# Kernel tuning notes

Hardware: AMD Instinct MI355X
Metric: run time of the kernel (lower is better)

Reference implementation:

```python
import jax, jax.numpy as jnp
import numpy as np

L, N, E, H, D = 2048, 4, 1024, 16, 128  # seq, batch, embed, heads, proj_dim
HD = E // H                             # head_dim = 64
SIGMA = 1.0
EPS = 1e-6


def setup_inputs() -> dict:
    key = jax.random.key(0)
    ks = jax.random.split(key, 13)
    w = lambda i, shape: jax.random.normal(ks[i], shape, jnp.float32) * 0.02
    return {
        "query": jax.random.normal(ks[0], (L, N, E), jnp.float32),
        "key": jax.random.normal(ks[1], (L, N, E), jnp.float32),
        "value": jax.random.normal(ks[2], (L, N, E), jnp.float32),
        "wq": w(3, (E, E)), "bq": jnp.zeros((E,), jnp.float32),
        "wk": w(4, (E, E)), "bk": jnp.zeros((E,), jnp.float32),
        "wv": w(5, (E, E)), "bv": jnp.zeros((E,), jnp.float32),
        "wo": w(6, (E, E)), "bo": jnp.zeros((E,), jnp.float32),
        "random_matrices": SIGMA * jax.random.normal(ks[7], (H, D, HD), jnp.float32),
    }


def random_project(x, rm):
    # x: (L, N, H, HD), rm: (H, D, HD) -> phi: (N*H, L, 2D)
    scale = 1.0 / np.sqrt(2 * D).astype(np.float32)
    xn = x / jnp.maximum(jnp.linalg.norm(x, axis=-1, keepdims=True), 1e-12)
    xt = jnp.einsum('lnhe,hde->lnhd', xn, rm)
    phi = scale * jnp.concatenate([jnp.exp(xt), jnp.exp(-xt)], axis=-1)  # (L,N,H,2D)
    # faithful to torch .contiguous().view(-1, L, 2D): plain row-major reshape
    return phi.reshape(N * H, L, 2 * D)


def causal_product(phi_q, phi_k, v):
    # phi_q, phi_k: (B, L, 2D); v: (B, L, HD)
    B = phi_q.shape[0]
    def step(carry, inp):
        S, z = carry            # S: (B, 2D, HD) running kv; z: (B, 2D) running k-sum
        qk, kk, vv = inp        # (B, 2D), (B, 2D), (B, HD)
        S = S + kk[:, :, None] * vv[:, None, :]
        z = z + kk
        num = jnp.einsum('bd,bdh->bh', qk, S)
        den = jnp.einsum('bd,bd->b', qk, z)
        return (S, z), num / (den[:, None] + EPS)
    init = (jnp.zeros((B, 2 * D, HD), phi_q.dtype), jnp.zeros((B, 2 * D), phi_q.dtype))
    xs = (jnp.swapaxes(phi_q, 0, 1), jnp.swapaxes(phi_k, 0, 1), jnp.swapaxes(v, 0, 1))
    _, out = jax.lax.scan(step, init, xs)   # out: (L, B, HD)
    return jnp.swapaxes(out, 0, 1)          # (B, L, HD)


def reference(query, key, value, wq, bq, wk, bk, wv, bv, wo, bo, random_matrices):
    q = query @ wq.T + bq
    k = key @ wk.T + bk
    v = value @ wv.T + bv
    q = q.reshape(L, N, H, HD)
    k = k.reshape(L, N, H, HD)
    v = jnp.swapaxes(v.reshape(L, N * H, HD), 0, 1)   # (B=N*H, L, HD)
    phi_q = random_project(q, random_matrices)        # (B, L, 2D)
    phi_k = random_project(k, random_matrices)
    attn = causal_product(phi_q, phi_k, v)            # (B, L, HD)
    attn = jnp.swapaxes(attn, 0, 1).reshape(L, N, E)
    return attn @ wo.T + bo
```

## Files before the change

### kernel.cpp

```cpp
#include <hip/hip_runtime.h>
#include <math.h>


typedef unsigned short u16;
typedef unsigned int u32;
using f32x4v  = __attribute__((ext_vector_type(4))) float;
using f32x16v = __attribute__((ext_vector_type(16))) float;
using s16x8   = __attribute__((ext_vector_type(8))) short;

__device__ __forceinline__ float bf2f(u16 u) { return __uint_as_float(((u32)u) << 16); }
__device__ __forceinline__ u16 f2bf(float x) {
    u32 b = __float_as_uint(x);
    b += 0x7fff + ((b >> 16) & 1);
    return (u16)(b >> 16);
}
__device__ __forceinline__ u32 cvtpk(float lo, float hi) {
    u32 r;
    asm("v_cvt_pk_bf16_f32 %0, %1, %2" : "=v"(r) : "v"(lo), "v"(hi));
    return r;
}
__device__ __forceinline__ float exp2f_hw(float x) {
    float r;
    asm("v_exp_f32 %0, %1" : "=v"(r) : "v"(x));
    return r;
}
__device__ __forceinline__ void gload_lds16(const void* g, void* l) {
    __builtin_amdgcn_global_load_lds(
        (const __attribute__((address_space(1))) void*)g,
        (__attribute__((address_space(3))) void*)l, 16, 0, 0);
}

__global__ __launch_bounds__(256) void cvt_consts(
    const float* __restrict__ w0, const float* __restrict__ w1,
    const float* __restrict__ w2, const float* __restrict__ w3,
    const float* __restrict__ rm, const float* __restrict__ query,
    const float* __restrict__ key, u16* __restrict__ wqkv,
    u16* __restrict__ wob, u16* __restrict__ rmb,
    u16* __restrict__ xq, u16* __restrict__ xk)
{
    const int y = blockIdx.y;
    const float* src;
    u16* d;
    int nblk;
    switch (y) {
        case 0: src = w0; d = wqkv;            nblk = 512;  break;
        case 1: src = w1; d = wqkv + 1048576;  nblk = 512;  break;
        case 2: src = w2; d = wqkv + 2097152;  nblk = 512;  break;
        case 3: src = w3; d = wob;             nblk = 512;  break;
        case 4: src = rm; d = rmb;             nblk = 64;   break;
        case 5: src = query; d = xq;           nblk = 4096; break;
        default: src = key; d = xk;            nblk = 4096; break;
    }
    if ((int)blockIdx.x >= nblk) return;
    const size_t i = ((size_t)blockIdx.x * 256 + threadIdx.x) * 8;
    const float4 a = *(const float4*)(src + i);
    const float4 b = *(const float4*)(src + i + 4);
    u16 o[8] = {f2bf(a.x), f2bf(a.y), f2bf(a.z), f2bf(a.w),
                f2bf(b.x), f2bf(b.y), f2bf(b.z), f2bf(b.w)};
    *(uint4*)(d + i) = *(uint4*)o;
}

__global__ __launch_bounds__(256) void gemm_qkv(
    const u16* __restrict__ XQ, const u16* __restrict__ XK, const float* __restrict__ Xv,
    const u16* __restrict__ WB, const float* __restrict__ bq, const float* __restrict__ bk,
    const float* __restrict__ bv, u16* __restrict__ qp, u16* __restrict__ kp, u16* __restrict__ vpt)
{
    __shared__ __align__(16) u16 As[4096];
    __shared__ __align__(16) u16 Bs[4096];
    const int z = blockIdx.z;
    const u16* Bw = WB + (size_t)z * 1048576;
    const float* bias = (z == 0) ? bq : (z == 1) ? bk : bv;

    const int t = threadIdx.x;
    const int m0 = blockIdx.x * 128, n0 = blockIdx.y * 128;
    const int wid = t >> 6, lane = t & 63;
    const int wr = wid >> 1, wc = wid & 1;
    const int l15 = lane & 15, l4 = lane >> 4;

    f32x4v acc[4][4];
#pragma unroll
    for (int i = 0; i < 4; ++i)
#pragma unroll
        for (int j = 0; j < 4; ++j)
#pragma unroll
            for (int e = 0; e < 4; ++e) acc[i][j][e] = 0.f;

    const int brow = wid * 32 + (lane >> 2);
    const int xr   = (brow >> 1) & 3;
    const int scol2 = (((lane & 3) ^ xr)) * 8;
    const u16* gb0 = Bw + (size_t)(n0 + brow) * 1024 + scol2;
    const u16* gb1 = gb0 + 16 * 1024;
    u16* lb0 = &Bs[wid * 1024];
    u16* lb1 = lb0 + 512;
    const u16* XA = (z == 0) ? XQ : XK;
    const u16* ga0 = XA + (size_t)(m0 + brow) * 1024 + scol2;
    const u16* ga1 = ga0 + 16 * 1024;
    u16* la0 = &As[wid * 1024];
    u16* la1 = la0 + 512;
    const int srow = t >> 1;
    const int scol = (t & 1) * 16;
    const int sx   = (srow >> 1) & 3;
    const int sl0  = (t & 1) * 2;
    u16* wa0 = &As[srow * 32 + ((sl0     ^ sx)) * 8];
    u16* wa1 = &As[srow * 32 + (((sl0+1) ^ sx)) * 8];
    const float* gsrcA = Xv + (size_t)(m0 + srow) * 1024 + scol;

    for (int k0 = 0; k0 < 1024; k0 += 32) {
        __syncthreads();
        gload_lds16(gb0 + k0, lb0);
        gload_lds16(gb1 + k0, lb1);
        if (z < 2) {
            gload_lds16(ga0 + k0, la0);
            gload_lds16(ga1 + k0, la1);
        } else {
            u16 ta[16];
#pragma unroll
            for (int q = 0; q < 4; ++q) {
                const float4 v = *(const float4*)(gsrcA + k0 + q * 4);
                ta[q*4+0] = f2bf(v.x); ta[q*4+1] = f2bf(v.y);
                ta[q*4+2] = f2bf(v.z); ta[q*4+3] = f2bf(v.w);
            }
            *(uint4*)wa0 = *(const uint4*)&ta[0];
            *(uint4*)wa1 = *(const uint4*)&ta[8];
        }
        __syncthreads();
        s16x8 af[4], bfr[4];
#pragma unroll
        for (int fi = 0; fi < 4; ++fi) {
            const int r  = wr * 64 + fi * 16 + l15;
            const int sl = l4 ^ ((r >> 1) & 3);
            af[fi] = *(const s16x8*)&As[r * 32 + sl * 8];
        }
#pragma unroll
        for (int fj = 0; fj < 4; ++fj) {
            const int r  = wc * 64 + fj * 16 + l15;
            const int sl = l4 ^ ((r >> 1) & 3);
            bfr[fj] = *(const s16x8*)&Bs[r * 32 + sl * 8];
        }
#pragma unroll
        for (int fi = 0; fi < 4; ++fi)
#pragma unroll
            for (int fj = 0; fj < 4; ++fj)
                acc[fi][fj] = __builtin_amdgcn_mfma_f32_16x16x32_bf16(af[fi], bfr[fj], acc[fi][fj], 0, 0, 0);
    }

    u16* Cp = (z == 0) ? qp : (z == 1) ? kp : vpt;
    const int rl = l4 * 4, cl = l15;
    float bvals[4];
#pragma unroll
    for (int fj = 0; fj < 4; ++fj) bvals[fj] = bias[n0 + wc * 64 + fj * 16 + cl];
#pragma unroll
    for (int fi = 0; fi < 4; ++fi)
#pragma unroll
        for (int j = 0; j < 4; ++j) {
            const size_t m = m0 + wr * 64 + fi * 16 + rl + j;
#pragma unroll
            for (int fj = 0; fj < 4; ++fj) {
                const int n = n0 + wc * 64 + fj * 16 + cl;
                const float v = acc[fi][fj][j] + bvals[fj];
                if (z < 2) Cp[m * 1024 + n] = f2bf(v);
                else       Cp[((size_t)((m & 3) * 16 + (n >> 6)) * 64 + (n & 63)) * 2048 + (m >> 2)] = f2bf(v);
            }
        }
}

__global__ __launch_bounds__(256) void gemm_o(
    const u16* __restrict__ A, const u16* __restrict__ Bw,
    const float* __restrict__ bias, float* __restrict__ Cp)
{
    __shared__ __align__(16) u16 As[4096];
    __shared__ __align__(16) u16 Bs[4096];
    const int t = threadIdx.x;
    const int m0 = blockIdx.x * 128, n0 = blockIdx.y * 128;
    const int wid = t >> 6, lane = t & 63;
    const int wr = wid >> 1, wc = wid & 1;
    const int l15 = lane & 15, l4 = lane >> 4;

    f32x4v acc[4][4];
#pragma unroll
    for (int i = 0; i < 4; ++i)
#pragma unroll
        for (int j = 0; j < 4; ++j)
#pragma unroll
            for (int e = 0; e < 4; ++e) acc[i][j][e] = 0.f;

    const int brow = wid * 32 + (lane >> 2);
    const int xr   = (brow >> 1) & 3;
    const int scol2 = (((lane & 3) ^ xr)) * 8;
    const u16* ga0 = A  + (size_t)(m0 + brow) * 1024 + scol2;
    const u16* ga1 = ga0 + 16 * 1024;
    const u16* gb0 = Bw + (size_t)(n0 + brow) * 1024 + scol2;
    const u16* gb1 = gb0 + 16 * 1024;
    u16* la0 = &As[wid * 1024];
    u16* la1 = la0 + 512;
    u16* lb0 = &Bs[wid * 1024];
    u16* lb1 = lb0 + 512;

    for (int k0 = 0; k0 < 1024; k0 += 32) {
        __syncthreads();
        gload_lds16(ga0 + k0, la0);
        gload_lds16(ga1 + k0, la1);
        gload_lds16(gb0 + k0, lb0);
        gload_lds16(gb1 + k0, lb1);
        __syncthreads();
        s16x8 af[4], bfr[4];
#pragma unroll
        for (int fi = 0; fi < 4; ++fi) {
            const int r  = wr * 64 + fi * 16 + l15;
            const int sl = l4 ^ ((r >> 1) & 3);
            af[fi] = *(const s16x8*)&As[r * 32 + sl * 8];
        }
#pragma unroll
        for (int fj = 0; fj < 4; ++fj) {
            const int r  = wc * 64 + fj * 16 + l15;
            const int sl = l4 ^ ((r >> 1) & 3);
            bfr[fj] = *(const s16x8*)&Bs[r * 32 + sl * 8];
        }
#pragma unroll
        for (int fi = 0; fi < 4; ++fi)
#pragma unroll
            for (int fj = 0; fj < 4; ++fj)
                acc[fi][fj] = __builtin_amdgcn_mfma_f32_16x16x32_bf16(af[fi], bfr[fj], acc[fi][fj], 0, 0, 0);
    }

    const int rl = l4 * 4, cl = l15;
    float bvals[4];
#pragma unroll
    for (int fj = 0; fj < 4; ++fj) bvals[fj] = bias[n0 + wc * 64 + fj * 16 + cl];
#pragma unroll
    for (int fi = 0; fi < 4; ++fi)
#pragma unroll
        for (int j = 0; j < 4; ++j) {
            const size_t m = m0 + wr * 64 + fi * 16 + rl + j;
#pragma unroll
            for (int fj = 0; fj < 4; ++fj) {
                const int n = n0 + wc * 64 + fj * 16 + cl;
                Cp[m * 1024 + n] = acc[fi][fj][j] + bvals[fj];
            }
        }
}

__global__ __launch_bounds__(256) void rand_project_mfma(
    const u16* __restrict__ QP, const u16* __restrict__ KP,
    const u16* __restrict__ RMB, u16* __restrict__ PHIQ, u16* __restrict__ PHIK)
{
    const u16* X  = (blockIdx.z == 0) ? QP : KP;
    u16* PHI      = (blockIdx.z == 0) ? PHIQ : PHIK;
    __shared__ __align__(16) u16 Xs[128 * 72];
    __shared__ __align__(16) u16 RMs[128 * 72];
    __shared__ float rsl_lds[128];
    const int h  = blockIdx.x;
    const int r0 = blockIdx.y * 128;
    const int t  = threadIdx.x;
    const int w  = t >> 6, lane = t & 63;
    const int l15 = lane & 15, l4 = lane >> 4;

    float sq[4];
#pragma unroll
    for (int i = 0; i < 4; ++i) {
        const int lin = t + i * 256;
        const int row = lin >> 3, oct = lin & 7;
        const uint4 xv = *(const uint4*)(X + (size_t)(r0 + row) * 1024 + h * 64 + oct * 8);
        *(uint4*)&Xs[row * 72 + oct * 8] = xv;
        const u16* pv = (const u16*)&xv;
        float s = 0.f;
#pragma unroll
        for (int e = 0; e < 8; ++e) { const float f = bf2f(pv[e]); s += f * f; }
        sq[i] = s;
        const uint4 rv = *(const uint4*)(RMB + (size_t)h * 8192 + lin * 8);
        *(uint4*)&RMs[row * 72 + oct * 8] = rv;
    }
#pragma unroll
    for (int i = 0; i < 4; ++i) {
        sq[i] += __shfl_xor(sq[i], 1);
        sq[i] += __shfl_xor(sq[i], 2);
        sq[i] += __shfl_xor(sq[i], 4);
        if ((t & 7) == 0)
            rsl_lds[(t >> 3) + i * 32] = 1.4426950408889634f / fmaxf(sqrtf(sq[i]), 1e-12f);
    }
    __syncthreads();

    const int wr = (w >> 1) * 64, wc = (w & 1) * 64;
    f32x4v acc[4][4];
#pragma unroll
    for (int i = 0; i < 4; ++i)
#pragma unroll
        for (int j = 0; j < 4; ++j)
#pragma unroll
            for (int e = 0; e < 4; ++e) acc[i][j][e] = 0.f;
#pragma unroll
    for (int ks = 0; ks < 2; ++ks) {
        s16x8 af[4], bfr[4];
#pragma unroll
        for (int fi = 0; fi < 4; ++fi)
            af[fi] = *(const s16x8*)&Xs[(wr + fi * 16 + l15) * 72 + ks * 32 + l4 * 8];
#pragma unroll
        for (int fj = 0; fj < 4; ++fj)
            bfr[fj] = *(const s16x8*)&RMs[(wc + fj * 16 + l15) * 72 + ks * 32 + l4 * 8];
#pragma unroll
        for (int fi = 0; fi < 4; ++fi)
#pragma unroll
            for (int fj = 0; fj < 4; ++fj)
                acc[fi][fj] = __builtin_amdgcn_mfma_f32_16x16x32_bf16(af[fi], bfr[fj], acc[fi][fj], 0, 0, 0);
    }

#pragma unroll
    for (int fi = 0; fi < 4; ++fi)
#pragma unroll
        for (int reg = 0; reg < 4; ++reg) {
            const int row = wr + fi * 16 + l4 * 4 + reg;
            const float rsl = rsl_lds[row];
            const size_t base = ((size_t)(r0 + row) * 16 + h) * 256;
#pragma unroll
            for (int fj = 0; fj < 4; ++fj) {
                const int d = wc + fj * 16 + l15;
                const float arg = acc[fi][fj][reg] * rsl;
                PHI[base + d]       = f2bf(exp2f_hw(arg - 4.f));
                PHI[base + 128 + d] = f2bf(exp2f_hw(-arg - 4.f));
            }
        }
}

__global__ __launch_bounds__(256) void chunk_state_mfma(
    const u16* __restrict__ PHIK, const u16* __restrict__ VPT, u16* __restrict__ STC)
{
    __shared__ __align__(16) u16 Ks[64 * 136];
    __shared__ float zlds[16][132];
    const int b = blockIdx.x;
    const int c = blockIdx.y >> 1;
    const int dh = blockIdx.y & 1;
    const int t = threadIdx.x;
    const int wid = t >> 6, lane = t & 63;
    const int l15 = lane & 15, l4 = lane >> 4;
    const int wr = wid >> 1, wc = wid & 1;

    const size_t R0 = (size_t)b * 2048 + (size_t)c * 256;
    const int rgrp = t >> 4, d08 = (t & 15) * 8;

    float zpart[8];
#pragma unroll
    for (int i = 0; i < 8; ++i) zpart[i] = 0.f;

    f32x4v acc[2][4];
#pragma unroll
    for (int i = 0; i < 2; ++i)
#pragma unroll
        for (int j = 0; j < 4; ++j)
#pragma unroll
            for (int e = 0; e < 4; ++e) acc[i][j][e] = 0.f;

    for (int stage = 0; stage < 4; ++stage) {
        __syncthreads();
#pragma unroll
        for (int j = 0; j < 4; ++j) {
            const int r = rgrp + 16 * j;
            const uint4 v = *(const uint4*)(PHIK + (R0 + stage * 64 + r) * 256 + dh * 128 + d08);
            const int x = ((r >> 3) & 3) << 1;
            *(uint4*)&Ks[r * 136 + (((d08 >> 3) ^ x) << 3)] = v;
            const u16* pv = (const u16*)&v;
#pragma unroll
            for (int i = 0; i < 8; ++i) zpart[i] += bf2f(pv[i]);
        }
        __syncthreads();
#pragma unroll
        for (int ks = 0; ks < 2; ++ks) {
            const int xk = ((ks * 4 + l4) & 3) << 1;
            const int r0 = ks * 32 + l4 * 8;
            s16x8 af[2], bk[4];
#pragma unroll
            for (int fi = 0; fi < 2; ++fi) {
                const int h = wr * 32 + fi * 16 + l15;
                af[fi] = *(const s16x8*)(VPT + ((size_t)b * 64 + h) * 2048 + c * 256 + stage * 64 + ks * 32 + l4 * 8);
            }
#pragma unroll
            for (int fj = 0; fj < 4; ++fj) {
                const int d = wc * 64 + fj * 16 + l15;
                const int colk = (((d >> 3) ^ xk) << 3) + (d & 7);
#pragma unroll
                for (int e = 0; e < 8; ++e)
                    bk[fj][e] = (short)Ks[(r0 + e) * 136 + colk];
            }
#pragma unroll
            for (int fi = 0; fi < 2; ++fi)
#pragma unroll
                for (int fj = 0; fj < 4; ++fj)
                    acc[fi][fj] = __builtin_amdgcn_mfma_f32_16x16x32_bf16(af[fi], bk[fj], acc[fi][fj], 0, 0, 0);
        }
    }
    __syncthreads();
    *(float4*)&zlds[rgrp][d08]     = *(float4*)&zpart[0];
    *(float4*)&zlds[rgrp][d08 + 4] = *(float4*)&zpart[4];
    __syncthreads();
    u16* st = STC + (size_t)(b * 8 + c) * 16640;
    if (t < 128) {
        float z = 0.f;
#pragma unroll
        for (int g = 0; g < 16; ++g) z += zlds[g][t];
        st[16384 + dh * 128 + t] = f2bf(z);
    }
#pragma unroll
    for (int fi = 0; fi < 2; ++fi)
#pragma unroll
        for (int reg = 0; reg < 4; ++reg) {
            const int h = wr * 32 + fi * 16 + l4 * 4 + reg;
#pragma unroll
            for (int fj = 0; fj < 4; ++fj) {
                const int d = dh * 128 + wc * 64 + fj * 16 + l15;
                st[(size_t)h * 256 + d] = f2bf(acc[fi][fj][reg]);
            }
        }
}

__global__ void prefix_scan(const u16* __restrict__ STC, u16* __restrict__ STBF)
{
    const int b = blockIdx.x;
    const int e = blockIdx.y * 256 + threadIdx.x;
    if (e >= 16640) return;
    float run = 0.f;
#pragma unroll
    for (int c = 0; c < 8; ++c) {
        const size_t idx = (size_t)(b * 8 + c) * 16640 + e;
        const float v = bf2f(STC[idx]);
        STBF[idx] = f2bf(run);
        run += v;
    }
}

__global__ __launch_bounds__(128) void causal_fused(
    const u16* __restrict__ PHIQ, const u16* __restrict__ PHIK,
    const u16* __restrict__ VPT, const u16* __restrict__ STBF,
    u16* __restrict__ ATT)
{
    const u32 bid = blockIdx.x;
    const int pair = (int)((bid >> 3) & 3);
    const int G  = (int)((bid >> 5) * 8 + (bid & 7));
    const int b  = G & 63;
    const int c  = G >> 6;
    const int w  = threadIdx.x >> 6;
    const int rf = w ? (7 - pair) : pair;
    const int ri = rf >> 1, fi = rf & 1;
    const int lane = threadIdx.x & 63;
    const int l31 = lane & 31, s = lane >> 5;
    const size_t chunk0 = (size_t)b * 2048 + (size_t)c * 256;
    const u16* stb = STBF + (size_t)(b * 8 + c) * 16640;

    const int qc = ri * 64 + fi * 32 + l31;
    s16x8 qf[16];
    const u16* qp = PHIQ + (chunk0 + qc) * 256 + s * 8;
#pragma unroll
    for (int ds = 0; ds < 16; ++ds)
        qf[ds] = *(const s16x8*)(qp + ds * 16);

    f32x16v o[2], o2;
#pragma unroll
    for (int e = 0; e < 16; ++e) { o[0][e] = 0.f; o[1][e] = 0.f; o2[e] = 0.f; }
    float den = 0.f;

#pragma unroll
    for (int ds = 0; ds < 16; ++ds) {
        const s16x8 zf = *(const s16x8*)(stb + 16384 + ds * 16 + s * 8);
        o2 = __builtin_amdgcn_mfma_f32_32x32x16_bf16(qf[ds], zf, o2, 0, 0, 0);
#pragma unroll
        for (int fh = 0; fh < 2; ++fh) {
            const s16x8 sx = *(const s16x8*)(stb + (fh * 32 + l31) * 256 + ds * 16 + s * 8);
            o[fh] = __builtin_amdgcn_mfma_f32_32x32x16_bf16(qf[ds], sx, o[fh], 0, 0, 0);
        }
    }

    const int kbmax = ri * 2 + fi;
    for (int kb = 0; kb <= kbmax; ++kb) {
        s16x8 vf[2][2];
#pragma unroll
        for (int kh = 0; kh < 2; ++kh)
#pragma unroll
            for (int fh = 0; fh < 2; ++fh)
                vf[kh][fh] = *(const s16x8*)(VPT + ((size_t)b * 64 + fh * 32 + l31) * 2048
                                             + c * 256 + kb * 32 + kh * 16 + s * 8);
        f32x16v p0, p1;
#pragma unroll
        for (int e = 0; e < 16; ++e) { p0[e] = 0.f; p1[e] = 0.f; }
        const u16* kptr = PHIK + (chunk0 + kb * 32 + l31) * 256 + s * 8;
#pragma unroll
        for (int ds = 0; ds < 8; ++ds) {
            const s16x8 kf0 = *(const s16x8*)(kptr + (2 * ds) * 16);
            const s16x8 kf1 = *(const s16x8*)(kptr + (2 * ds + 1) * 16);
            p0 = __builtin_amdgcn_mfma_f32_32x32x16_bf16(kf0, qf[2 * ds],     p0, 0, 0, 0);
            p1 = __builtin_amdgcn_mfma_f32_32x32x16_bf16(kf1, qf[2 * ds + 1], p1, 0, 0, 0);
        }
        f32x16v p;
#pragma unroll
        for (int e = 0; e < 16; ++e) p[e] = p0[e] + p1[e];

        const bool diag = (kb == kbmax);
        float rsum = 0.f;
#pragma unroll
        for (int reg = 0; reg < 16; ++reg) {
            if (diag) {
                const int kc = kb * 32 + (reg & 3) + 8 * (reg >> 2) + 4 * s;
                if (kc > qc) p[reg] = 0.f;
            }
            rsum += p[reg];
        }
        den += rsum;
#pragma unroll
        for (int kh = 0; kh < 2; ++kh) {
            const u32 pA_lo = cvtpk(p[8*kh + 0], p[8*kh + 1]);
            const u32 pA_hi = cvtpk(p[8*kh + 2], p[8*kh + 3]);
            const u32 pB_lo = cvtpk(p[8*kh + 4], p[8*kh + 5]);
            const u32 pB_hi = cvtpk(p[8*kh + 6], p[8*kh + 7]);
            const u32 X_lo = s ? pB_lo : pA_lo;
            const u32 X_hi = s ? pB_hi : pA_hi;
            const u32 Y_lo = s ? pA_lo : pB_lo;
            const u32 Y_hi = s ? pA_hi : pB_hi;
            const u32 sY_lo = __shfl_xor((int)Y_lo, 32);
            const u32 sY_hi = __shfl_xor((int)Y_hi, 32);
            u32 wq[4];
            wq[0] = s ? sY_lo : X_lo;
            wq[1] = s ? sY_hi : X_hi;
            wq[2] = s ? X_lo : sY_lo;
            wq[3] = s ? X_hi : sY_hi;
            s16x8 pa;
#pragma unroll
            for (int i = 0; i < 4; ++i) {
                pa[2*i]   = (short)(wq[i] & 0xffff);
                pa[2*i+1] = (short)(wq[i] >> 16);
            }
            o[0] = __builtin_amdgcn_mfma_f32_32x32x16_bf16(pa, vf[kh][0], o[0], 0, 0, 0);
            o[1] = __builtin_amdgcn_mfma_f32_32x32x16_bf16(pa, vf[kh][1], o[1], 0, 0, 0);
        }
    }

    const float denT = den + __shfl_xor(den, 32);
#pragma unroll
    for (int reg = 0; reg < 16; ++reg) {
        const int q32 = (reg & 3) + 8 * (reg >> 2) + 4 * s;
        const float dv = o2[reg] + __shfl(denT, q32);
        const float inv = 1.f / (dv + 1e-6f);
        const int qrow = c * 256 + ri * 64 + fi * 32 + q32;
        const size_t abase = (size_t)qrow * 4096 + b * 64;
        ATT[abase + l31]      = f2bf(o[0][reg] * inv);
        ATT[abase + 32 + l31] = f2bf(o[1][reg] * inv);
    }
}

extern "C" void kernel_launch(void* const* d_in, const int* in_sizes, int n_in,
                              void* d_out, int out_size, void* d_ws, size_t ws_size,
                              hipStream_t stream)
{
    const float* query = (const float*)d_in[0];
    const float* key   = (const float*)d_in[1];
    const float* value = (const float*)d_in[2];
    const float* wq    = (const float*)d_in[3];
    const float* bq    = (const float*)d_in[4];
    const float* wk    = (const float*)d_in[5];
    const float* bk    = (const float*)d_in[6];
    const float* wv    = (const float*)d_in[7];
    const float* bv    = (const float*)d_in[8];
    const float* wo    = (const float*)d_in[9];
    const float* bo    = (const float*)d_in[10];
    const float* rm    = (const float*)d_in[11];
    float* out = (float*)d_out;

    char* base = (char*)d_ws;
    u16* phiq = (u16*)(base);
    u16* phik = (u16*)(base +  67108864);
    u16* vpt  = (u16*)(base + 134217728);
    u16* qp   = (u16*)(base + 150994944);
    u16* kp   = (u16*)(base + 167772160);
    u16* stc  = (u16*)(base + 184549376);
    u16* stbf = (u16*)(base + 201588736);
    u16* xq   = (u16*)(base + 184549376);
    u16* xk   = (u16*)(base + 201326592);
    u16* wob  = (u16*)(base + 218628096);
    u16* rmb  = (u16*)(base + 220725248);
    u16* wqkv = phiq;
    u16* attn = qp;

    const dim3 blk(256);
    cvt_consts<<<dim3(4096, 7), blk, 0, stream>>>(wq, wk, wv, wo, rm, query, key,
                                                  wqkv, wob, rmb, xq, xk);
    gemm_qkv<<<dim3(64, 8, 3), blk, 0, stream>>>(xq, xk, value, wqkv, bq, bk, bv, qp, kp, vpt);
    rand_project_mfma<<<dim3(16, 64, 2), blk, 0, stream>>>(qp, kp, rmb, phiq, phik);
    chunk_state_mfma<<<dim3(64, 16), blk, 0, stream>>>(phik, vpt, stc);
    prefix_scan<<<dim3(64, 65), blk, 0, stream>>>(stc, stbf);
    causal_fused<<<dim3(2048), dim3(128), 0, stream>>>(phiq, phik, vpt, stbf, attn);
    gemm_o<<<dim3(64, 8), blk, 0, stream>>>(attn, wob, bo, out);
}
```

Before: 285.7 us.

## Double-buffer LDS tiles in QKV and output projection GEMMs

Both projection GEMM kernels now keep two LDS buffers for the A and B tiles. Each iteration issues the loads for the next k-tile into the other buffer before running MFMAs on the current one, and only one barrier remains per iteration. The goal is to hide global-to-LDS latency behind matrix math. In exchange LDS use per block doubles to 32KB, which may lower occupancy. The async LDS loads also rely on the end-of-iteration barrier for completion, so correctness depends on that barrier waiting for them.

Result: no change. 290.9 us (+1.8%).

```diff
diff --git a/kernel.cpp b/kernel.cpp
--- a/kernel.cpp
+++ b/kernel.cpp
@@ -65,8 +65,8 @@
     const u16* __restrict__ WB, const float* __restrict__ bq, const float* __restrict__ bk,
     const float* __restrict__ bv, u16* __restrict__ qp, u16* __restrict__ kp, u16* __restrict__ vpt)
 {
-    __shared__ __align__(16) u16 As[4096];
-    __shared__ __align__(16) u16 Bs[4096];
+    __shared__ __align__(16) u16 As[2][4096];
+    __shared__ __align__(16) u16 Bs[2][4096];
     const int z = blockIdx.z;
     const u16* Bw = WB + (size_t)z * 1048576;
     const float* bias = (z == 0) ? bq : (z == 1) ? bk : bv;
@@ -88,60 +88,73 @@
     const int brow = wid * 32 + (lane >> 2);
     const int xr   = (brow >> 1) & 3;
     const int scol2 = (((lane & 3) ^ xr)) * 8;
-    const u16* gb0 = Bw + (size_t)(n0 + brow) * 1024 + scol2;
-    const u16* gb1 = gb0 + 16 * 1024;
-    u16* lb0 = &Bs[wid * 1024];
-    u16* lb1 = lb0 + 512;
+    const u16* gb = Bw + (size_t)(n0 + brow) * 1024 + scol2;
     const u16* XA = (z == 0) ? XQ : XK;
-    const u16* ga0 = XA + (size_t)(m0 + brow) * 1024 + scol2;
-    const u16* ga1 = ga0 + 16 * 1024;
-    u16* la0 = &As[wid * 1024];
-    u16* la1 = la0 + 512;
+    const u16* ga = XA + (size_t)(m0 + brow) * 1024 + scol2;
     const int srow = t >> 1;
     const int scol = (t & 1) * 16;
     const int sx   = (srow >> 1) & 3;
     const int sl0  = (t & 1) * 2;
-    u16* wa0 = &As[srow * 32 + ((sl0     ^ sx)) * 8];
-    u16* wa1 = &As[srow * 32 + (((sl0+1) ^ sx)) * 8];
     const float* gsrcA = Xv + (size_t)(m0 + srow) * 1024 + scol;
 
-    for (int k0 = 0; k0 < 1024; k0 += 32) {
-        __syncthreads();
-        gload_lds16(gb0 + k0, lb0);
-        gload_lds16(gb1 + k0, lb1);
-        if (z < 2) {
-            gload_lds16(ga0 + k0, la0);
-            gload_lds16(ga1 + k0, la1);
-        } else {
-            u16 ta[16];
-#pragma unroll
-            for (int q = 0; q < 4; ++q) {
-                const float4 v = *(const float4*)(gsrcA + k0 + q * 4);
-                ta[q*4+0] = f2bf(v.x); ta[q*4+1] = f2bf(v.y);
-                ta[q*4+2] = f2bf(v.z); ta[q*4+3] = f2bf(v.w);
-            }
-            *(uint4*)wa0 = *(const uint4*)&ta[0];
-            *(uint4*)wa1 = *(const uint4*)&ta[8];
-        }
-        __syncthreads();
+    gload_lds16(gb, &Bs[0][wid * 1024]);
+    gload_lds16(gb + 16 * 1024, &Bs[0][wid * 1024 + 512]);
+    if (z < 2) {
+        gload_lds16(ga, &As[0][wid * 1024]);
+        gload_lds16(ga + 16 * 1024, &As[0][wid * 1024 + 512]);
+    } else {
+        u16 ta[16];
+#pragma unroll
+        for (int q = 0; q < 4; ++q) {
+            const float4 v = *(const float4*)(gsrcA + q * 4);
+            ta[q*4+0] = f2bf(v.x); ta[q*4+1] = f2bf(v.y);
+            ta[q*4+2] = f2bf(v.z); ta[q*4+3] = f2bf(v.w);
+        }
+        *(uint4*)&As[0][srow * 32 + ((sl0     ^ sx)) * 8] = *(const uint4*)&ta[0];
+        *(uint4*)&As[0][srow * 32 + (((sl0+1) ^ sx)) * 8] = *(const uint4*)&ta[8];
+    }
+    __syncthreads();
+
+    for (int k = 0; k < 32; ++k) {
+        const int cur = k & 1;
+        if (k < 31) {
+            const int nk0 = (k + 1) * 32;
+            gload_lds16(gb + nk0, &Bs[cur ^ 1][wid * 1024]);
+            gload_lds16(gb + 16 * 1024 + nk0, &Bs[cur ^ 1][wid * 1024 + 512]);
+            if (z < 2) {
+                gload_lds16(ga + nk0, &As[cur ^ 1][wid * 1024]);
+                gload_lds16(ga + 16 * 1024 + nk0, &As[cur ^ 1][wid * 1024 + 512]);
+            } else {
+                u16 ta[16];
+#pragma unroll
+                for (int q = 0; q < 4; ++q) {
+                    const float4 v = *(const float4*)(gsrcA + nk0 + q * 4);
+                    ta[q*4+0] = f2bf(v.x); ta[q*4+1] = f2bf(v.y);
+                    ta[q*4+2] = f2bf(v.z); ta[q*4+3] = f2bf(v.w);
+                }
+                *(uint4*)&As[cur ^ 1][srow * 32 + ((sl0     ^ sx)) * 8] = *(const uint4*)&ta[0];
+                *(uint4*)&As[cur ^ 1][srow * 32 + (((sl0+1) ^ sx)) * 8] = *(const uint4*)&ta[8];
+            }
+        }
         s16x8 af[4], bfr[4];
 #pragma unroll
         for (int fi = 0; fi < 4; ++fi) {
             const int r  = wr * 64 + fi * 16 + l15;
             const int sl = l4 ^ ((r >> 1) & 3);
-            af[fi] = *(const s16x8*)&As[r * 32 + sl * 8];
+            af[fi] = *(const s16x8*)&As[cur][r * 32 + sl * 8];
         }
 #pragma unroll
         for (int fj = 0; fj < 4; ++fj) {
             const int r  = wc * 64 + fj * 16 + l15;
             const int sl = l4 ^ ((r >> 1) & 3);
-            bfr[fj] = *(const s16x8*)&Bs[r * 32 + sl * 8];
+            bfr[fj] = *(const s16x8*)&Bs[cur][r * 32 + sl * 8];
         }
 #pragma unroll
         for (int fi = 0; fi < 4; ++fi)
 #pragma unroll
             for (int fj = 0; fj < 4; ++fj)
                 acc[fi][fj] = __builtin_amdgcn_mfma_f32_16x16x32_bf16(af[fi], bfr[fj], acc[fi][fj], 0, 0, 0);
+        __syncthreads();
     }
 
     u16* Cp = (z == 0) ? qp : (z == 1) ? kp : vpt;
@@ -168,8 +181,8 @@
     const u16* __restrict__ A, const u16* __restrict__ Bw,
     const float* __restrict__ bias, float* __restrict__ Cp)
 {
-    __shared__ __align__(16) u16 As[4096];
-    __shared__ __align__(16) u16 Bs[4096];
+    __shared__ __align__(16) u16 As[2][4096];
+    __shared__ __align__(16) u16 Bs[2][4096];
     const int t = threadIdx.x;
     const int m0 = blockIdx.x * 128, n0 = blockIdx.y * 128;
     const int wid = t >> 6, lane = t & 63;
@@ -187,40 +200,43 @@
     const int brow = wid * 32 + (lane >> 2);
     const int xr   = (brow >> 1) & 3;
     const int scol2 = (((lane & 3) ^ xr)) * 8;
-    const u16* ga0 = A  + (size_t)(m0 + brow) * 1024 + scol2;
-    const u16* ga1 = ga0 + 16 * 1024;
-    const u16* gb0 = Bw + (size_t)(n0 + brow) * 1024 + scol2;
-    const u16* gb1 = gb0 + 16 * 1024;
-    u16* la0 = &As[wid * 1024];
-    u16* la1 = la0 + 512;
-    u16* lb0 = &Bs[wid * 1024];
-    u16* lb1 = lb0 + 512;
-
-    for (int k0 = 0; k0 < 1024; k0 += 32) {
-        __syncthreads();
-        gload_lds16(ga0 + k0, la0);
-        gload_lds16(ga1 + k0, la1);
-        gload_lds16(gb0 + k0, lb0);
-        gload_lds16(gb1 + k0, lb1);
-        __syncthreads();
+    const u16* ga = A  + (size_t)(m0 + brow) * 1024 + scol2;
+    const u16* gb = Bw + (size_t)(n0 + brow) * 1024 + scol2;
+
+    gload_lds16(ga, &As[0][wid * 1024]);
+    gload_lds16(ga + 16 * 1024, &As[0][wid * 1024 + 512]);
+    gload_lds16(gb, &Bs[0][wid * 1024]);
+    gload_lds16(gb + 16 * 1024, &Bs[0][wid * 1024 + 512]);
+    __syncthreads();
+
+    for (int k = 0; k < 32; ++k) {
+        const int cur = k & 1;
+        if (k < 31) {
+            const int nk0 = (k + 1) * 32;
+            gload_lds16(ga + nk0, &As[cur ^ 1][wid * 1024]);
+            gload_lds16(ga + 16 * 1024 + nk0, &As[cur ^ 1][wid * 1024 + 512]);
+            gload_lds16(gb + nk0, &Bs[cur ^ 1][wid * 1024]);
+            gload_lds16(gb + 16 * 1024 + nk0, &Bs[cur ^ 1][wid * 1024 + 512]);
+        }
         s16x8 af[4], bfr[4];
 #pragma unroll
         for (int fi = 0; fi < 4; ++fi) {
             const int r  = wr * 64 + fi * 16 + l15;
             const int sl = l4 ^ ((r >> 1) & 3);
-            af[fi] = *(const s16x8*)&As[r * 32 + sl * 8];
+            af[fi] = *(const s16x8*)&As[cur][r * 32 + sl * 8];
         }
 #pragma unroll
         for (int fj = 0; fj < 4; ++fj) {
             const int r  = wc * 64 + fj * 16 + l15;
             const int sl = l4 ^ ((r >> 1) & 3);
-            bfr[fj] = *(const s16x8*)&Bs[r * 32 + sl * 8];
+            bfr[fj] = *(const s16x8*)&Bs[cur][r * 32 + sl * 8];
         }
 #pragma unroll
         for (int fi = 0; fi < 4; ++fi)
 #pragma unroll
             for (int fj = 0; fj < 4; ++fj)
                 acc[fi][fj] = __builtin_amdgcn_mfma_f32_16x16x32_bf16(af[fi], bfr[fj], acc[fi][fj], 0, 0, 0);
+        __syncthreads();
     }
 
     const int rl = l4 * 4, cl = l15;
```
